# Performance work log

Measured on AMD Instinct MI355X. Metric: run time of the kernel, lower is better.

The kernel has to match this reference:

```python
import jax, jax.numpy as jnp
import numpy as np

B, D, A, R = 256, 1024, 1024, 8  # batch, feat_dim, ada_dim, rank
I = A  # inter_dim defaults to ada_dim
LN_EPS = 1e-5


def setup_inputs() -> dict:
    key = jax.random.key(0)
    ks = jax.random.split(key, 5)
    return {
        "x": jax.random.normal(ks[0], (B, D), jnp.float32),
        "ada_emb": jax.random.normal(ks[1], (B, A), jnp.float32),
        "base_layer": jax.random.normal(ks[2], (D, D), jnp.float32) * 0.02,
        "ln_gamma": jnp.ones((A,), jnp.float32),
        "ln_beta": jnp.zeros((A,), jnp.float32),
        "W1": jax.random.normal(ks[3], (A, I), jnp.float32) * 0.02,
        "b1": jnp.zeros((I,), jnp.float32),
        "W2": jax.random.normal(ks[4], (I, D * R * 2), jnp.float32) * 0.02,
        "b2": jnp.zeros((D * R * 2,), jnp.float32),
    }


def reference(x, ada_emb, base_layer, ln_gamma, ln_beta, W1, b1, W2, b2):
    Bc, Dc = x.shape
    # norm_cond: LayerNorm over ada_dim
    mu = jnp.mean(ada_emb, axis=-1, keepdims=True)
    var = jnp.var(ada_emb, axis=-1, keepdims=True)
    cond = (ada_emb - mu) * jax.lax.rsqrt(var + LN_EPS) * ln_gamma + ln_beta
    # gen_weight: Linear -> GELU (exact, erf) -> Linear
    h = jax.nn.gelu(cond @ W1 + b1, approximate=False)
    w = h @ W2 + b2                      # [B, 2*D*R]
    x_a, x_b = jnp.split(w, 2, axis=-1)
    x_a = x_a.reshape(Bc, Dc, R)         # [B, D, R]
    x_b = x_b.reshape(Bc, Dc, R)         # [B, D, R]
    # per-sample low-rank weight added to the shared base layer
    layer = base_layer[None, :, :] + jnp.einsum('bdr,bkr->bdk', x_a, x_b)  # [B, D, D]
    out = jnp.einsum('bc,bco->bo', x, layer)
    return x + out  # residual=True
```

## Files before the change

### kernel.cpp

```cpp
#include <hip/hip_runtime.h>
#include <math.h>

#define BB 256
#define DD 1024
#define AA 1024
#define RR 8
#define II 1024
#define NOUT (2*DD*RR)
#define LN_EPS 1e-5f

typedef __attribute__((ext_vector_type(8))) short bf16x8;
typedef __attribute__((ext_vector_type(4))) float f32x4;

typedef const __attribute__((address_space(1))) unsigned int gu32_t;
typedef __attribute__((address_space(3))) unsigned int lu32_t;

__device__ __forceinline__ void glds16(void* lds, const void* g) {
    __builtin_amdgcn_global_load_lds((gu32_t*)g, (lu32_t*)lds, 16, 0, 0);
}

__device__ __forceinline__ f32x4 mfma16(bf16x8 a, bf16x8 b, f32x4 c) {
    return __builtin_amdgcn_mfma_f32_16x16x32_bf16(a, b, c, 0, 0, 0);
}

__device__ __forceinline__ unsigned short f2bf(float x) {
    unsigned int u = __float_as_uint(x);
    unsigned int r = (u + 0x7fffu + ((u >> 16) & 1u)) >> 16;
    return (unsigned short)r;
}
__device__ __forceinline__ float bf2f(unsigned short b) {
    return __uint_as_float(((unsigned int)b) << 16);
}
__device__ __forceinline__ void split2(float x, unsigned short& hi, unsigned short& lo) {
    hi = f2bf(x);
    lo = f2bf(x - bf2f(hi));
}

__device__ __forceinline__ float gelu_exact(float v) {
    return 0.5f * v * (1.0f + erff(v * 0.70710678118654752f));
}

__global__ __launch_bounds__(256) void ln_split_kernel(const float* __restrict__ ada,
                                                       const float* __restrict__ xp,
                                                       const float* __restrict__ gamma,
                                                       const float* __restrict__ beta,
                                                       unsigned short* __restrict__ c_hi,
                                                       unsigned short* __restrict__ c_lo,
                                                       unsigned short* __restrict__ x_hi,
                                                       unsigned short* __restrict__ x_lo) {
    const int b = blockIdx.x;
    const int tid = threadIdx.x;
    const float4 v = ((const float4*)(ada + (size_t)b * AA))[tid];

    float s  = v.x + v.y + v.z + v.w;
    float ss = v.x * v.x + v.y * v.y + v.z * v.z + v.w * v.w;
    #pragma unroll
    for (int off = 32; off; off >>= 1) {
        s  += __shfl_down(s, off);
        ss += __shfl_down(ss, off);
    }
    __shared__ float red[2][4];
    const int wid = tid >> 6, lane = tid & 63;
    if (lane == 0) { red[0][wid] = s; red[1][wid] = ss; }
    __syncthreads();
    __shared__ float stats[2];
    if (tid == 0) {
        float S  = red[0][0] + red[0][1] + red[0][2] + red[0][3];
        float SS = red[1][0] + red[1][1] + red[1][2] + red[1][3];
        float mu  = S * (1.0f / AA);
        float var = SS * (1.0f / AA) - mu * mu;
        stats[0] = mu;
        stats[1] = rsqrtf(var + LN_EPS);
    }
    __syncthreads();
    const float mu = stats[0], inv = stats[1];
    const float4 g  = ((const float4*)gamma)[tid];
    const float4 be = ((const float4*)beta)[tid];
    float o[4];
    o[0] = (v.x - mu) * inv * g.x + be.x;
    o[1] = (v.y - mu) * inv * g.y + be.y;
    o[2] = (v.z - mu) * inv * g.z + be.z;
    o[3] = (v.w - mu) * inv * g.w + be.w;
    ushort4 H, L;
    split2(o[0], H.x, L.x); split2(o[1], H.y, L.y);
    split2(o[2], H.z, L.z); split2(o[3], H.w, L.w);
    ((ushort4*)(c_hi + (size_t)b * AA))[tid] = H;
    ((ushort4*)(c_lo + (size_t)b * AA))[tid] = L;

    const float4 xv = ((const float4*)(xp + (size_t)b * DD))[tid];
    split2(xv.x, H.x, L.x); split2(xv.y, H.y, L.y);
    split2(xv.z, H.z, L.z); split2(xv.w, H.w, L.w);
    ((ushort4*)(x_hi + (size_t)b * DD))[tid] = H;
    ((ushort4*)(x_lo + (size_t)b * DD))[tid] = L;
}

__global__ __launch_bounds__(256) void gemm_small(const unsigned short* __restrict__ x_hi,
                                                  const unsigned short* __restrict__ x_lo,
                                                  const unsigned short* __restrict__ c_hi,
                                                  const unsigned short* __restrict__ c_lo,
                                                  const float* __restrict__ base,
                                                  const float* __restrict__ W1,
                                                  const float* __restrict__ b1,
                                                  float* __restrict__ outy,
                                                  unsigned short* __restrict__ h_hi,
                                                  unsigned short* __restrict__ h_lo) {
    __shared__ __align__(16) unsigned short As[2][4096];
    __shared__ __align__(16) unsigned short Bs[2][4096];

    const int z = blockIdx.z;
    const unsigned short* __restrict__ Ahi = z ? c_hi : x_hi;
    const unsigned short* __restrict__ Alo = z ? c_lo : x_lo;
    const float* __restrict__ Bsrc = z ? W1 : base;

    const int tid = threadIdx.x;
    const int bn = blockIdx.x * 64;
    const int bm = blockIdx.y * 64;
    const int wid = tid >> 6, l = tid & 63;
    const int wm = wid >> 1, wn = wid & 1;
    const int kg = l >> 4;
    const int lr16 = (l & 15) * 16;

    f32x4 acc[2][2];
    #pragma unroll
    for (int i = 0; i < 2; i++)
        #pragma unroll
        for (int j = 0; j < 2; j++) acc[i][j] = (f32x4)0.0f;

    const int sn = l;
    const int skq = (tid >> 6) << 2;
    const int s_nblk = sn >> 4, s_lr16 = (sn & 15) * 16;

    float v[8];
    #pragma unroll
    for (int h = 0; h < 2; h++)
        #pragma unroll
        for (int i = 0; i < 4; i++)
            v[h * 4 + i] = Bsrc[(size_t)(skq + 16 * h + i) * 1024 + bn + sn];
    #pragma unroll
    for (int i = 0; i < 2; i++) {
        const int ch = wid * 2 + i;
        const unsigned short* src = (ch < 4) ? Ahi : Alo;
        const int row = bm + (ch & 3) * 16 + (l & 15);
        glds16((char*)As[0] + ch * 1024, src + (size_t)row * 1024 + kg * 8);
    }
    #pragma unroll
    for (int h = 0; h < 2; h++) {
        ushort4 H, L;
        split2(v[h*4+0], H.x, L.x); split2(v[h*4+1], H.y, L.y);
        split2(v[h*4+2], H.z, L.z); split2(v[h*4+3], H.w, L.w);
        const int kbyte = (skq + 16 * h) * 2;
        const int kch = kbyte >> 4, low = kbyte & 15;
        *(ushort4*)((char*)Bs[0] + ((0 * 4 + s_nblk) * 4 + kch) * 256 + s_lr16 + low) = H;
        *(ushort4*)((char*)Bs[0] + ((1 * 4 + s_nblk) * 4 + kch) * 256 + s_lr16 + low) = L;
    }
    __syncthreads();

    int cur = 0;
    for (int t = 0; t < 32; ++t) {
        const bool pf = (t < 31);
        const int k0n = (t + 1) * 32;
        if (pf) {
            #pragma unroll
            for (int h = 0; h < 2; h++)
                #pragma unroll
                for (int i = 0; i < 4; i++)
                    v[h * 4 + i] = Bsrc[(size_t)(k0n + skq + 16 * h + i) * 1024 + bn + sn];
            #pragma unroll
            for (int i = 0; i < 2; i++) {
                const int ch = wid * 2 + i;
                const unsigned short* src = (ch < 4) ? Ahi : Alo;
                const int row = bm + (ch & 3) * 16 + (l & 15);
                glds16((char*)As[cur ^ 1] + ch * 1024, src + (size_t)row * 1024 + k0n + kg * 8);
            }
        }
        {
            bf16x8 a[2][2], bb[2][2];
            #pragma unroll
            for (int pl = 0; pl < 2; pl++) {
                #pragma unroll
                for (int mi = 0; mi < 2; mi++)
                    a[pl][mi] = *(const bf16x8*)((const char*)As[cur] +
                        ((pl * 4 + wm * 2 + mi) * 4 + kg) * 256 + lr16);
                #pragma unroll
                for (int ni = 0; ni < 2; ni++)
                    bb[pl][ni] = *(const bf16x8*)((const char*)Bs[cur] +
                        ((pl * 4 + wn * 2 + ni) * 4 + kg) * 256 + lr16);
            }
            #pragma unroll
            for (int mi = 0; mi < 2; mi++)
                #pragma unroll
                for (int ni = 0; ni < 2; ni++) {
                    acc[mi][ni] = mfma16(a[0][mi], bb[0][ni], acc[mi][ni]);
                    acc[mi][ni] = mfma16(a[0][mi], bb[1][ni], acc[mi][ni]);
                    acc[mi][ni] = mfma16(a[1][mi], bb[0][ni], acc[mi][ni]);
                }
        }
        if (pf) {
            #pragma unroll
            for (int h = 0; h < 2; h++) {
                ushort4 H, L;
                split2(v[h*4+0], H.x, L.x); split2(v[h*4+1], H.y, L.y);
                split2(v[h*4+2], H.z, L.z); split2(v[h*4+3], H.w, L.w);
                const int kbyte = (skq + 16 * h) * 2;
                const int kch = kbyte >> 4, low = kbyte & 15;
                *(ushort4*)((char*)Bs[cur ^ 1] + ((0 * 4 + s_nblk) * 4 + kch) * 256 + s_lr16 + low) = H;
                *(ushort4*)((char*)Bs[cur ^ 1] + ((1 * 4 + s_nblk) * 4 + kch) * 256 + s_lr16 + low) = L;
            }
        }
        __syncthreads();
        cur ^= 1;
    }

    #pragma unroll
    for (int mi = 0; mi < 2; mi++) {
        #pragma unroll
        for (int ni = 0; ni < 2; ni++) {
            const int row0 = bm + wm * 32 + mi * 16 + kg * 4;
            const int col  = bn + wn * 32 + ni * 16 + (l & 15);
            #pragma unroll
            for (int j = 0; j < 4; j++) {
                float val = acc[mi][ni][j];
                if (z == 0) {
                    outy[(size_t)(row0 + j) * 1024 + col] = val;
                } else {
                    float g = gelu_exact(val + b1[col]);
                    unsigned short hi, lo;
                    split2(g, hi, lo);
                    h_hi[(size_t)(row0 + j) * 1024 + col] = hi;
                    h_lo[(size_t)(row0 + j) * 1024 + col] = lo;
                }
            }
        }
    }
}

__global__ __launch_bounds__(512) void gemm_big(const unsigned short* __restrict__ Ahi,
                                                const unsigned short* __restrict__ Alo,
                                                const float* __restrict__ Bm,
                                                const float* __restrict__ bias,
                                                float* __restrict__ Cm) {
    __shared__ __align__(16) unsigned short As[2][16384];
    __shared__ __align__(16) unsigned short Bs[2][4096];

    const int tid = threadIdx.x;
    const int bn  = blockIdx.x * 64;
    const int wid = tid >> 6, l = tid & 63;
    const int kg = l >> 4;
    const int lr16 = (l & 15) * 16;

    f32x4 acc[2][4];
    #pragma unroll
    for (int i = 0; i < 2; i++)
        #pragma unroll
        for (int j = 0; j < 4; j++) acc[i][j] = (f32x4)0.0f;

    const int sn = l;
    const int skq = wid * 4;
    const int s_nblk = sn >> 4, s_lr16 = (sn & 15) * 16;
    const int s_kbyte = skq * 2;
    const int s_kch = s_kbyte >> 4, s_low = s_kbyte & 15;

    float v[4];
    #pragma unroll
    for (int i = 0; i < 4; i++)
        v[i] = Bm[(size_t)(skq + i) * NOUT + bn + sn];
    #pragma unroll
    for (int i = 0; i < 4; i++) {
        const int ch = wid * 4 + i;
        const unsigned short* src = (ch < 16) ? Ahi : Alo;
        const int row = (ch & 15) * 16 + (l & 15);
        glds16((char*)As[0] + ch * 1024, src + (size_t)row * II + kg * 8);
    }
    {
        ushort4 H, L;
        split2(v[0], H.x, L.x); split2(v[1], H.y, L.y);
        split2(v[2], H.z, L.z); split2(v[3], H.w, L.w);
        *(ushort4*)((char*)Bs[0] + ((0 * 4 + s_nblk) * 4 + s_kch) * 256 + s_lr16 + s_low) = H;
        *(ushort4*)((char*)Bs[0] + ((1 * 4 + s_nblk) * 4 + s_kch) * 256 + s_lr16 + s_low) = L;
    }
    __syncthreads();

    int cur = 0;
    for (int t = 0; t < 32; ++t) {
        const bool pf = (t < 31);
        const int k0n = (t + 1) * 32;
        if (pf) {
            #pragma unroll
            for (int i = 0; i < 4; i++)
                v[i] = Bm[(size_t)(k0n + skq + i) * NOUT + bn + sn];
            #pragma unroll
            for (int i = 0; i < 4; i++) {
                const int ch = wid * 4 + i;
                const unsigned short* src = (ch < 16) ? Ahi : Alo;
                const int row = (ch & 15) * 16 + (l & 15);
                glds16((char*)As[cur ^ 1] + ch * 1024, src + (size_t)row * II + k0n + kg * 8);
            }
        }
        {
            bf16x8 a[2][2], bb[2][4];
            #pragma unroll
            for (int pl = 0; pl < 2; pl++) {
                #pragma unroll
                for (int mi = 0; mi < 2; mi++)
                    a[pl][mi] = *(const bf16x8*)((const char*)As[cur] +
                        ((pl * 16 + wid * 2 + mi) * 4 + kg) * 256 + lr16);
                #pragma unroll
                for (int ni = 0; ni < 4; ni++)
                    bb[pl][ni] = *(const bf16x8*)((const char*)Bs[cur] +
                        ((pl * 4 + ni) * 4 + kg) * 256 + lr16);
            }
            #pragma unroll
            for (int mi = 0; mi < 2; mi++)
                #pragma unroll
                for (int ni = 0; ni < 4; ni++) {
                    acc[mi][ni] = mfma16(a[0][mi], bb[0][ni], acc[mi][ni]);
                    acc[mi][ni] = mfma16(a[0][mi], bb[1][ni], acc[mi][ni]);
                    acc[mi][ni] = mfma16(a[1][mi], bb[0][ni], acc[mi][ni]);
                }
        }
        if (pf) {
            ushort4 H, L;
            split2(v[0], H.x, L.x); split2(v[1], H.y, L.y);
            split2(v[2], H.z, L.z); split2(v[3], H.w, L.w);
            *(ushort4*)((char*)Bs[cur ^ 1] + ((0 * 4 + s_nblk) * 4 + s_kch) * 256 + s_lr16 + s_low) = H;
            *(ushort4*)((char*)Bs[cur ^ 1] + ((1 * 4 + s_nblk) * 4 + s_kch) * 256 + s_lr16 + s_low) = L;
        }
        __syncthreads();
        cur ^= 1;
    }

    #pragma unroll
    for (int mi = 0; mi < 2; mi++) {
        #pragma unroll
        for (int ni = 0; ni < 4; ni++) {
            const int row0 = wid * 32 + mi * 16 + kg * 4;
            const int col  = bn + ni * 16 + (l & 15);
            const float bv = bias[col];
            #pragma unroll
            for (int j = 0; j < 4; j++)
                Cm[(size_t)(row0 + j) * NOUT + col] = acc[mi][ni][j] + bv;
        }
    }
}

__global__ __launch_bounds__(256) void t_kernel(const float* __restrict__ x,
                                                const float* __restrict__ w,
                                                float* __restrict__ tmat) {
    const int b = blockIdx.x;
    const int tid = threadIdx.x;
    const float* wa = w + (size_t)b * NOUT;
    const float4 xv = ((const float4*)(x + (size_t)b * DD))[tid];
    const float xs[4] = {xv.x, xv.y, xv.z, xv.w};

    float acc[RR] = {};
    #pragma unroll
    for (int i = 0; i < 4; i++) {
        const int c = tid * 4 + i;
        const float4 w0 = *(const float4*)&wa[c * RR];
        const float4 w1 = *(const float4*)&wa[c * RR + 4];
        acc[0] = fmaf(xs[i], w0.x, acc[0]);
        acc[1] = fmaf(xs[i], w0.y, acc[1]);
        acc[2] = fmaf(xs[i], w0.z, acc[2]);
        acc[3] = fmaf(xs[i], w0.w, acc[3]);
        acc[4] = fmaf(xs[i], w1.x, acc[4]);
        acc[5] = fmaf(xs[i], w1.y, acc[5]);
        acc[6] = fmaf(xs[i], w1.z, acc[6]);
        acc[7] = fmaf(xs[i], w1.w, acc[7]);
    }
    __shared__ float red[4][RR];
    const int wid = tid >> 6, lane = tid & 63;
    #pragma unroll
    for (int r = 0; r < RR; r++) {
        float vv = acc[r];
        #pragma unroll
        for (int off = 32; off; off >>= 1) vv += __shfl_down(vv, off);
        if (lane == 0) red[wid][r] = vv;
    }
    __syncthreads();
    if (tid < RR) {
        tmat[b * RR + tid] = red[0][tid] + red[1][tid] + red[2][tid] + red[3][tid];
    }
}

__global__ __launch_bounds__(256) void final_kernel(const float* __restrict__ x,
                                                    const float* __restrict__ w,
                                                    const float* __restrict__ tmat,
                                                    float* __restrict__ out) {
    const int b = blockIdx.x;
    const int tid = threadIdx.x;
    float tr[RR];
    #pragma unroll
    for (int r = 0; r < RR; r++) tr[r] = tmat[b * RR + r];

    const float* wb = w + (size_t)b * NOUT + DD * RR;
    const int o0 = tid * 4;
    const float4 xv = *(const float4*)&x[(size_t)b * DD + o0];
    const float4 yv = *(const float4*)&out[(size_t)b * DD + o0];

    float vals[4];
    #pragma unroll
    for (int i = 0; i < 4; i++) {
        const float4 w0 = *(const float4*)&wb[(o0 + i) * RR];
        const float4 w1 = *(const float4*)&wb[(o0 + i) * RR + 4];
        vals[i] = tr[0] * w0.x + tr[1] * w0.y + tr[2] * w0.z + tr[3] * w0.w
                + tr[4] * w1.x + tr[5] * w1.y + tr[6] * w1.z + tr[7] * w1.w;
    }
    float4 o;
    o.x = xv.x + yv.x + vals[0];
    o.y = xv.y + yv.y + vals[1];
    o.z = xv.z + yv.z + vals[2];
    o.w = xv.w + yv.w + vals[3];
    *(float4*)&out[(size_t)b * DD + o0] = o;
}

extern "C" void kernel_launch(void* const* d_in, const int* in_sizes, int n_in,
                              void* d_out, int out_size, void* d_ws, size_t ws_size,
                              hipStream_t stream) {
    const float* x     = (const float*)d_in[0];
    const float* ada   = (const float*)d_in[1];
    const float* base  = (const float*)d_in[2];
    const float* gamma = (const float*)d_in[3];
    const float* beta  = (const float*)d_in[4];
    const float* W1    = (const float*)d_in[5];
    const float* b1    = (const float*)d_in[6];
    const float* W2    = (const float*)d_in[7];
    const float* b2    = (const float*)d_in[8];
    float* out = (float*)d_out;

    char* wsb = (char*)d_ws;
    float* w = (float*)(wsb);
    unsigned short* h_hi = (unsigned short*)(wsb + 16777216);
    unsigned short* h_lo = (unsigned short*)(wsb + 17301504);
    unsigned short* x_hi = (unsigned short*)(wsb + 17825792);
    unsigned short* x_lo = (unsigned short*)(wsb + 18350080);
    unsigned short* c_hi = (unsigned short*)(wsb + 18874368);
    unsigned short* c_lo = (unsigned short*)(wsb + 19398656);
    float* tmat = (float*)(wsb + 19922944);

    ln_split_kernel<<<BB, 256, 0, stream>>>(ada, x, gamma, beta, c_hi, c_lo, x_hi, x_lo);

    gemm_small<<<dim3(DD / 64, BB / 64, 2), 256, 0, stream>>>(
        x_hi, x_lo, c_hi, c_lo, base, W1, b1, out, h_hi, h_lo);

    gemm_big<<<dim3(NOUT / 64, 1), 512, 0, stream>>>(h_hi, h_lo, W2, b2, w);

    t_kernel<<<BB, 256, 0, stream>>>(x, w, tmat);

    final_kernel<<<BB, 256, 0, stream>>>(x, w, tmat, out);
}
```

Baseline: 208.1 us.

## Retile both GEMMs and fuse the rank-reduction and final kernels

gemm_small switches to 32x64 tiles with a K step of 64, which doubles its grid. gemm_big moves from 64-wide full-batch tiles with 512 threads to 128x128 tiles with 256 threads and a 4x4 MFMA register block per wave. t_kernel and final_kernel become a single tail_kernel that keeps the per-sample rank vector in shared memory, removing one launch and the tmat round trip through global memory. The larger register tiles raise register pressure and could lower occupancy.

```diff
diff --git a/kernel.cpp b/kernel.cpp
--- a/kernel.cpp
+++ b/kernel.cpp
@@ -105,7 +105,7 @@
                                                   unsigned short* __restrict__ h_hi,
                                                   unsigned short* __restrict__ h_lo) {
     __shared__ __align__(16) unsigned short As[2][4096];
-    __shared__ __align__(16) unsigned short Bs[2][4096];
+    __shared__ __align__(16) unsigned short Bs[2][8192];
 
     const int z = blockIdx.z;
     const unsigned short* __restrict__ Ahi = z ? c_hi : x_hi;
@@ -114,238 +114,243 @@
 
     const int tid = threadIdx.x;
     const int bn = blockIdx.x * 64;
-    const int bm = blockIdx.y * 64;
+    const int bm = blockIdx.y * 32;
+    const int wid = tid >> 6, l = tid & 63;
+    const int wn = wid;
+    const int kg = l >> 4;
+    const int lr16 = (l & 15) * 16;
+
+    f32x4 acc[2];
+    acc[0] = (f32x4)0.0f; acc[1] = (f32x4)0.0f;
+
+    const int sn = tid & 63;
+    const int s_nb = sn >> 4, s_lane16 = (sn & 15) * 16;
+    const int s_k4 = (tid >> 6) * 4;
+
+    float v[4][4];
+
+    #define SB_LOAD(K0)                                                         \
+        _Pragma("unroll")                                                       \
+        for (int p = 0; p < 4; p++) {                                           \
+            const int kq = s_k4 + p * 16;                                       \
+            _Pragma("unroll")                                                   \
+            for (int i = 0; i < 4; i++)                                         \
+                v[p][i] = Bsrc[(size_t)((K0) + kq + i) * 1024 + bn + sn];       \
+        }
+
+    #define SB_WRITE(BUF)                                                       \
+        _Pragma("unroll")                                                       \
+        for (int p = 0; p < 4; p++) {                                           \
+            const int kq = s_k4 + p * 16;                                       \
+            const int kidx = kq >> 3, klow2 = (kq & 7) * 2;                     \
+            ushort4 H, L;                                                       \
+            split2(v[p][0], H.x, L.x); split2(v[p][1], H.y, L.y);               \
+            split2(v[p][2], H.z, L.z); split2(v[p][3], H.w, L.w);               \
+            *(ushort4*)((char*)Bs[BUF] + ((0*4 + s_nb)*8 + kidx)*256 + s_lane16 + klow2) = H; \
+            *(ushort4*)((char*)Bs[BUF] + ((1*4 + s_nb)*8 + kidx)*256 + s_lane16 + klow2) = L; \
+        }
+
+    #define SA_GLDS(BUF, K0)                                                    \
+        _Pragma("unroll")                                                       \
+        for (int c = 0; c < 2; c++) {                                           \
+            const int ch = wid * 2 + c;                               \
+            const int pl = ch >> 2, rr = ch & 3;                                \
+            const int m = rr & 1, half = rr >> 1;                               \
+            const unsigned short* src = (pl ? Alo : Ahi)                        \
+                + (size_t)(bm + m * 16 + (l & 15)) * 1024 + (K0) + half * 32 + kg * 8; \
+            glds16((char*)As[BUF] + ((pl*2 + m)*8 + half*4) * 256, src);        \
+        }
+
+    #define S_COMPUTE(BUF)                                                      \
+        {                                                                       \
+            _Pragma("unroll")                                                   \
+            for (int s = 0; s < 2; s++) {                                       \
+                bf16x8 a[2][2], bbf[2];                                         \
+                _Pragma("unroll")                                               \
+                for (int pl = 0; pl < 2; pl++) {                                \
+                    _Pragma("unroll")                                           \
+                    for (int mi = 0; mi < 2; mi++)                              \
+                        a[pl][mi] = *(const bf16x8*)((const char*)As[BUF] +     \
+                            ((pl*2 + mi)*8 + s*4 + kg)*256 + lr16);             \
+                    bbf[pl] = *(const bf16x8*)((const char*)Bs[BUF] +           \
+                            ((pl*4 + wn)*8 + s*4 + kg)*256 + lr16);             \
+                }                                                               \
+                _Pragma("unroll")                                               \
+                for (int mi = 0; mi < 2; mi++) {                                \
+                    acc[mi] = mfma16(a[0][mi], bbf[0], acc[mi]);                \
+                    acc[mi] = mfma16(a[0][mi], bbf[1], acc[mi]);                \
+                    acc[mi] = mfma16(a[1][mi], bbf[0], acc[mi]);                \
+                }                                                               \
+            }                                                                   \
+        }
+
+    SB_LOAD(0);
+    SA_GLDS(0, 0);
+    SB_WRITE(0);
+    __syncthreads();
+
+    int cur = 0;
+    for (int t = 0; t < 16; ++t) {
+        if (t < 15) {
+            const int k0n = (t + 1) * 64;
+            SB_LOAD(k0n);
+            SA_GLDS(cur ^ 1, k0n);
+        }
+        S_COMPUTE(cur);
+        if (t < 15) {
+            SB_WRITE(cur ^ 1);
+            __syncthreads();
+        }
+        cur ^= 1;
+    }
+
+    #pragma unroll
+    for (int mi = 0; mi < 2; mi++) {
+        const int row0 = bm + mi * 16 + (l >> 4) * 4;
+        const int col  = bn + wn * 16 + (l & 15);
+        #pragma unroll
+        for (int j = 0; j < 4; j++) {
+            float val = acc[mi][j];
+            if (z == 0) {
+                outy[(size_t)(row0 + j) * 1024 + col] = val;
+            } else {
+                float g = gelu_exact(val + b1[col]);
+                unsigned short hi, lo;
+                split2(g, hi, lo);
+                h_hi[(size_t)(row0 + j) * 1024 + col] = hi;
+                h_lo[(size_t)(row0 + j) * 1024 + col] = lo;
+            }
+        }
+    }
+    #undef SB_LOAD
+    #undef SB_WRITE
+    #undef SA_GLDS
+    #undef S_COMPUTE
+}
+
+__global__ __launch_bounds__(256) void gemm_big(const unsigned short* __restrict__ Ahi,
+                                                const unsigned short* __restrict__ Alo,
+                                                const float* __restrict__ Bm,
+                                                const float* __restrict__ bias,
+                                                float* __restrict__ Cm) {
+    __shared__ __align__(16) unsigned short As[2][8192];
+    __shared__ __align__(16) unsigned short Bs[2][8192];
+
+    const int tid = threadIdx.x;
+    const int bn = blockIdx.x * 128;
+    const int bm = blockIdx.y * 128;
     const int wid = tid >> 6, l = tid & 63;
     const int wm = wid >> 1, wn = wid & 1;
     const int kg = l >> 4;
     const int lr16 = (l & 15) * 16;
 
-    f32x4 acc[2][2];
-    #pragma unroll
-    for (int i = 0; i < 2; i++)
+    f32x4 acc[4][4];
+    #pragma unroll
+    for (int i = 0; i < 4; i++)
         #pragma unroll
-        for (int j = 0; j < 2; j++) acc[i][j] = (f32x4)0.0f;
-
-    const int sn = l;
-    const int skq = (tid >> 6) << 2;
-    const int s_nblk = sn >> 4, s_lr16 = (sn & 15) * 16;
-
-    float v[8];
-    #pragma unroll
-    for (int h = 0; h < 2; h++)
-        #pragma unroll
-        for (int i = 0; i < 4; i++)
-            v[h * 4 + i] = Bsrc[(size_t)(skq + 16 * h + i) * 1024 + bn + sn];
-    #pragma unroll
-    for (int i = 0; i < 2; i++) {
-        const int ch = wid * 2 + i;
-        const unsigned short* src = (ch < 4) ? Ahi : Alo;
-        const int row = bm + (ch & 3) * 16 + (l & 15);
-        glds16((char*)As[0] + ch * 1024, src + (size_t)row * 1024 + kg * 8);
-    }
-    #pragma unroll
-    for (int h = 0; h < 2; h++) {
-        ushort4 H, L;
-        split2(v[h*4+0], H.x, L.x); split2(v[h*4+1], H.y, L.y);
-        split2(v[h*4+2], H.z, L.z); split2(v[h*4+3], H.w, L.w);
-        const int kbyte = (skq + 16 * h) * 2;
-        const int kch = kbyte >> 4, low = kbyte & 15;
-        *(ushort4*)((char*)Bs[0] + ((0 * 4 + s_nblk) * 4 + kch) * 256 + s_lr16 + low) = H;
-        *(ushort4*)((char*)Bs[0] + ((1 * 4 + s_nblk) * 4 + kch) * 256 + s_lr16 + low) = L;
-    }
+        for (int j = 0; j < 4; j++) acc[i][j] = (f32x4)0.0f;
+
+    const int sn = tid & 127;
+    const int s_nb = sn >> 4, s_lane16 = (sn & 15) * 16;
+    const int s_kb = (tid >> 7) * 4;
+
+    float v[4][4];
+
+    #define GB_LOAD(K0)                                                         \
+        _Pragma("unroll")                                                       \
+        for (int p = 0; p < 4; p++) {                                           \
+            const int kq = s_kb + p * 8;                                        \
+            _Pragma("unroll")                                                   \
+            for (int i = 0; i < 4; i++)                                         \
+                v[p][i] = Bm[(size_t)((K0) + kq + i) * NOUT + bn + sn];         \
+        }
+
+    #define GB_WRITE(BUF)                                                       \
+        _Pragma("unroll")                                                       \
+        for (int p = 0; p < 4; p++) {                                           \
+            ushort4 H, L;                                                       \
+            split2(v[p][0], H.x, L.x); split2(v[p][1], H.y, L.y);               \
+            split2(v[p][2], H.z, L.z); split2(v[p][3], H.w, L.w);               \
+            *(ushort4*)((char*)Bs[BUF] + ((0*8 + s_nb)*4 + p)*256 + s_lane16 + s_kb*2) = H; \
+            *(ushort4*)((char*)Bs[BUF] + ((1*8 + s_nb)*4 + p)*256 + s_lane16 + s_kb*2) = L; \
+        }
+
+    #define GA_GLDS(BUF, K0)                                                    \
+        _Pragma("unroll")                                                       \
+        for (int c = 0; c < 4; c++) {                                           \
+            const int ch = wid * 4 + c;                              \
+            const int pl = ch >> 3, m = ch & 7;                                 \
+            const unsigned short* src = (pl ? Alo : Ahi)                        \
+                + (size_t)(bm + m * 16 + (l & 15)) * II + (K0) + kg * 8;        \
+            glds16((char*)As[BUF] + ch * 1024, src);                            \
+        }
+
+    #define G_COMPUTE(BUF)                                                     \
+        {                                                                       \
+            bf16x8 a[2][4], bbf[2][4];                                          \
+            _Pragma("unroll")                                                   \
+            for (int pl = 0; pl < 2; pl++) {                                    \
+                _Pragma("unroll")                                               \
+                for (int mi = 0; mi < 4; mi++)                                  \
+                    a[pl][mi] = *(const bf16x8*)((const char*)As[BUF] +         \
+                        ((pl*8 + wm*4 + mi)*4 + kg)*256 + lr16);                \
+                _Pragma("unroll")                                               \
+                for (int ni = 0; ni < 4; ni++)                                  \
+                    bbf[pl][ni] = *(const bf16x8*)((const char*)Bs[BUF] +       \
+                        ((pl*8 + wn*4 + ni)*4 + kg)*256 + lr16);                \
+            }                                                                   \
+            _Pragma("unroll")                                                   \
+            for (int mi = 0; mi < 4; mi++) {                                    \
+                _Pragma("unroll")                                               \
+                for (int ni = 0; ni < 4; ni++) {                                \
+                    acc[mi][ni] = mfma16(a[0][mi], bbf[0][ni], acc[mi][ni]);    \
+                    acc[mi][ni] = mfma16(a[0][mi], bbf[1][ni], acc[mi][ni]);    \
+                    acc[mi][ni] = mfma16(a[1][mi], bbf[0][ni], acc[mi][ni]);    \
+                }                                                               \
+            }                                                                   \
+        }
+
+    GB_LOAD(0);
+    GA_GLDS(0, 0);
+    GB_WRITE(0);
     __syncthreads();
 
     int cur = 0;
     for (int t = 0; t < 32; ++t) {
-        const bool pf = (t < 31);
-        const int k0n = (t + 1) * 32;
-        if (pf) {
-            #pragma unroll
-            for (int h = 0; h < 2; h++)
-                #pragma unroll
-                for (int i = 0; i < 4; i++)
-                    v[h * 4 + i] = Bsrc[(size_t)(k0n + skq + 16 * h + i) * 1024 + bn + sn];
-            #pragma unroll
-            for (int i = 0; i < 2; i++) {
-                const int ch = wid * 2 + i;
-                const unsigned short* src = (ch < 4) ? Ahi : Alo;
-                const int row = bm + (ch & 3) * 16 + (l & 15);
-                glds16((char*)As[cur ^ 1] + ch * 1024, src + (size_t)row * 1024 + k0n + kg * 8);
-            }
-        }
-        {
-            bf16x8 a[2][2], bb[2][2];
-            #pragma unroll
-            for (int pl = 0; pl < 2; pl++) {
-                #pragma unroll
-                for (int mi = 0; mi < 2; mi++)
-                    a[pl][mi] = *(const bf16x8*)((const char*)As[cur] +
-                        ((pl * 4 + wm * 2 + mi) * 4 + kg) * 256 + lr16);
-                #pragma unroll
-                for (int ni = 0; ni < 2; ni++)
-                    bb[pl][ni] = *(const bf16x8*)((const char*)Bs[cur] +
-                        ((pl * 4 + wn * 2 + ni) * 4 + kg) * 256 + lr16);
-            }
-            #pragma unroll
-            for (int mi = 0; mi < 2; mi++)
-                #pragma unroll
-                for (int ni = 0; ni < 2; ni++) {
-                    acc[mi][ni] = mfma16(a[0][mi], bb[0][ni], acc[mi][ni]);
-                    acc[mi][ni] = mfma16(a[0][mi], bb[1][ni], acc[mi][ni]);
-                    acc[mi][ni] = mfma16(a[1][mi], bb[0][ni], acc[mi][ni]);
-                }
-        }
-        if (pf) {
-            #pragma unroll
-            for (int h = 0; h < 2; h++) {
-                ushort4 H, L;
-                split2(v[h*4+0], H.x, L.x); split2(v[h*4+1], H.y, L.y);
-                split2(v[h*4+2], H.z, L.z); split2(v[h*4+3], H.w, L.w);
-                const int kbyte = (skq + 16 * h) * 2;
-                const int kch = kbyte >> 4, low = kbyte & 15;
-                *(ushort4*)((char*)Bs[cur ^ 1] + ((0 * 4 + s_nblk) * 4 + kch) * 256 + s_lr16 + low) = H;
-                *(ushort4*)((char*)Bs[cur ^ 1] + ((1 * 4 + s_nblk) * 4 + kch) * 256 + s_lr16 + low) = L;
-            }
-        }
-        __syncthreads();
+        if (t < 31) {
+            const int k0n = (t + 1) * 32;
+            GB_LOAD(k0n);
+            GA_GLDS(cur ^ 1, k0n);
+        }
+        G_COMPUTE(cur);
+        if (t < 31) {
+            GB_WRITE(cur ^ 1);
+            __syncthreads();
+        }
         cur ^= 1;
     }
 
     #pragma unroll
-    for (int mi = 0; mi < 2; mi++) {
-        #pragma unroll
-        for (int ni = 0; ni < 2; ni++) {
-            const int row0 = bm + wm * 32 + mi * 16 + kg * 4;
-            const int col  = bn + wn * 32 + ni * 16 + (l & 15);
-            #pragma unroll
-            for (int j = 0; j < 4; j++) {
-                float val = acc[mi][ni][j];
-                if (z == 0) {
-                    outy[(size_t)(row0 + j) * 1024 + col] = val;
-                } else {
-                    float g = gelu_exact(val + b1[col]);
-                    unsigned short hi, lo;
-                    split2(g, hi, lo);
-                    h_hi[(size_t)(row0 + j) * 1024 + col] = hi;
-                    h_lo[(size_t)(row0 + j) * 1024 + col] = lo;
-                }
-            }
-        }
-    }
-}
-
-__global__ __launch_bounds__(512) void gemm_big(const unsigned short* __restrict__ Ahi,
-                                                const unsigned short* __restrict__ Alo,
-                                                const float* __restrict__ Bm,
-                                                const float* __restrict__ bias,
-                                                float* __restrict__ Cm) {
-    __shared__ __align__(16) unsigned short As[2][16384];
-    __shared__ __align__(16) unsigned short Bs[2][4096];
-
-    const int tid = threadIdx.x;
-    const int bn  = blockIdx.x * 64;
-    const int wid = tid >> 6, l = tid & 63;
-    const int kg = l >> 4;
-    const int lr16 = (l & 15) * 16;
-
-    f32x4 acc[2][4];
-    #pragma unroll
-    for (int i = 0; i < 2; i++)
-        #pragma unroll
-        for (int j = 0; j < 4; j++) acc[i][j] = (f32x4)0.0f;
-
-    const int sn = l;
-    const int skq = wid * 4;
-    const int s_nblk = sn >> 4, s_lr16 = (sn & 15) * 16;
-    const int s_kbyte = skq * 2;
-    const int s_kch = s_kbyte >> 4, s_low = s_kbyte & 15;
-
-    float v[4];
-    #pragma unroll
-    for (int i = 0; i < 4; i++)
-        v[i] = Bm[(size_t)(skq + i) * NOUT + bn + sn];
-    #pragma unroll
-    for (int i = 0; i < 4; i++) {
-        const int ch = wid * 4 + i;
-        const unsigned short* src = (ch < 16) ? Ahi : Alo;
-        const int row = (ch & 15) * 16 + (l & 15);
-        glds16((char*)As[0] + ch * 1024, src + (size_t)row * II + kg * 8);
-    }
-    {
-        ushort4 H, L;
-        split2(v[0], H.x, L.x); split2(v[1], H.y, L.y);
-        split2(v[2], H.z, L.z); split2(v[3], H.w, L.w);
-        *(ushort4*)((char*)Bs[0] + ((0 * 4 + s_nblk) * 4 + s_kch) * 256 + s_lr16 + s_low) = H;
-        *(ushort4*)((char*)Bs[0] + ((1 * 4 + s_nblk) * 4 + s_kch) * 256 + s_lr16 + s_low) = L;
-    }
-    __syncthreads();
-
-    int cur = 0;
-    for (int t = 0; t < 32; ++t) {
-        const bool pf = (t < 31);
-        const int k0n = (t + 1) * 32;
-        if (pf) {
-            #pragma unroll
-            for (int i = 0; i < 4; i++)
-                v[i] = Bm[(size_t)(k0n + skq + i) * NOUT + bn + sn];
-            #pragma unroll
-            for (int i = 0; i < 4; i++) {
-                const int ch = wid * 4 + i;
-                const unsigned short* src = (ch < 16) ? Ahi : Alo;
-                const int row = (ch & 15) * 16 + (l & 15);
-                glds16((char*)As[cur ^ 1] + ch * 1024, src + (size_t)row * II + k0n + kg * 8);
-            }
-        }
-        {
-            bf16x8 a[2][2], bb[2][4];
-            #pragma unroll
-            for (int pl = 0; pl < 2; pl++) {
-                #pragma unroll
-                for (int mi = 0; mi < 2; mi++)
-                    a[pl][mi] = *(const bf16x8*)((const char*)As[cur] +
-                        ((pl * 16 + wid * 2 + mi) * 4 + kg) * 256 + lr16);
-                #pragma unroll
-                for (int ni = 0; ni < 4; ni++)
-                    bb[pl][ni] = *(const bf16x8*)((const char*)Bs[cur] +
-                        ((pl * 4 + ni) * 4 + kg) * 256 + lr16);
-            }
-            #pragma unroll
-            for (int mi = 0; mi < 2; mi++)
-                #pragma unroll
-                for (int ni = 0; ni < 4; ni++) {
-                    acc[mi][ni] = mfma16(a[0][mi], bb[0][ni], acc[mi][ni]);
-                    acc[mi][ni] = mfma16(a[0][mi], bb[1][ni], acc[mi][ni]);
-                    acc[mi][ni] = mfma16(a[1][mi], bb[0][ni], acc[mi][ni]);
-                }
-        }
-        if (pf) {
-            ushort4 H, L;
-            split2(v[0], H.x, L.x); split2(v[1], H.y, L.y);
-            split2(v[2], H.z, L.z); split2(v[3], H.w, L.w);
-            *(ushort4*)((char*)Bs[cur ^ 1] + ((0 * 4 + s_nblk) * 4 + s_kch) * 256 + s_lr16 + s_low) = H;
-            *(ushort4*)((char*)Bs[cur ^ 1] + ((1 * 4 + s_nblk) * 4 + s_kch) * 256 + s_lr16 + s_low) = L;
-        }
-        __syncthreads();
-        cur ^= 1;
-    }
-
-    #pragma unroll
-    for (int mi = 0; mi < 2; mi++) {
+    for (int mi = 0; mi < 4; mi++) {
         #pragma unroll
         for (int ni = 0; ni < 4; ni++) {
-            const int row0 = wid * 32 + mi * 16 + kg * 4;
-            const int col  = bn + ni * 16 + (l & 15);
+            const int row0 = bm + wm * 64 + mi * 16 + (l >> 4) * 4;
+            const int col  = bn + wn * 64 + ni * 16 + (l & 15);
             const float bv = bias[col];
             #pragma unroll
             for (int j = 0; j < 4; j++)
                 Cm[(size_t)(row0 + j) * NOUT + col] = acc[mi][ni][j] + bv;
         }
     }
-}
-
-__global__ __launch_bounds__(256) void t_kernel(const float* __restrict__ x,
-                                                const float* __restrict__ w,
-                                                float* __restrict__ tmat) {
+    #undef GB_LOAD
+    #undef GB_WRITE
+    #undef GA_GLDS
+    #undef G_COMPUTE
+}
+
+__global__ __launch_bounds__(256) void tail_kernel(const float* __restrict__ x,
+                                                   const float* __restrict__ w,
+                                                   float* __restrict__ out) {
     const int b = blockIdx.x;
     const int tid = threadIdx.x;
     const float* wa = w + (size_t)b * NOUT;
@@ -368,6 +373,7 @@
         acc[7] = fmaf(xs[i], w1.w, acc[7]);
     }
     __shared__ float red[4][RR];
+    __shared__ float trs[RR];
     const int wid = tid >> 6, lane = tid & 63;
     #pragma unroll
     for (int r = 0; r < RR; r++) {
@@ -377,24 +383,15 @@
         if (lane == 0) red[wid][r] = vv;
     }
     __syncthreads();
-    if (tid < RR) {
-        tmat[b * RR + tid] = red[0][tid] + red[1][tid] + red[2][tid] + red[3][tid];
-    }
-}
-
-__global__ __launch_bounds__(256) void final_kernel(const float* __restrict__ x,
-                                                    const float* __restrict__ w,
-                                                    const float* __restrict__ tmat,
-                                                    float* __restrict__ out) {
-    const int b = blockIdx.x;
-    const int tid = threadIdx.x;
+    if (tid < RR) trs[tid] = red[0][tid] + red[1][tid] + red[2][tid] + red[3][tid];
+    __syncthreads();
+
     float tr[RR];
     #pragma unroll
-    for (int r = 0; r < RR; r++) tr[r] = tmat[b * RR + r];
-
-    const float* wb = w + (size_t)b * NOUT + DD * RR;
+    for (int r = 0; r < RR; r++) tr[r] = trs[r];
+
+    const float* wb = wa + DD * RR;
     const int o0 = tid * 4;
-    const float4 xv = *(const float4*)&x[(size_t)b * DD + o0];
     const float4 yv = *(const float4*)&out[(size_t)b * DD + o0];
 
     float vals[4];
@@ -435,16 +432,13 @@
     unsigned short* x_lo = (unsigned short*)(wsb + 18350080);
     unsigned short* c_hi = (unsigned short*)(wsb + 18874368);
     unsigned short* c_lo = (unsigned short*)(wsb + 19398656);
-    float* tmat = (float*)(wsb + 19922944);
 
     ln_split_kernel<<<BB, 256, 0, stream>>>(ada, x, gamma, beta, c_hi, c_lo, x_hi, x_lo);
 
-    gemm_small<<<dim3(DD / 64, BB / 64, 2), 256, 0, stream>>>(
+    gemm_small<<<dim3(1024 / 64, BB / 32, 2), 256, 0, stream>>>(
         x_hi, x_lo, c_hi, c_lo, base, W1, b1, out, h_hi, h_lo);
 
-    gemm_big<<<dim3(NOUT / 64, 1), 512, 0, stream>>>(h_hi, h_lo, W2, b2, w);
-
-    t_kernel<<<BB, 256, 0, stream>>>(x, w, tmat);
-
-    final_kernel<<<BB, 256, 0, stream>>>(x, w, tmat, out);
-}
+    gemm_big<<<dim3(NOUT / 128, BB / 128), 256, 0, stream>>>(h_hi, h_lo, W2, b2, w);
+
+    tail_kernel<<<BB, 256, 0, stream>>>(x, w, out);
+}
```

New measurement: 202.3 us. 1.03x faster.
